# Kernel optimization log

Hardware: AMD Instinct MI355X
Metric: run time of the kernel (lower is better)

Reference implementation:

```python
import jax, jax.numpy as jnp
import numpy as np

IMAGE_SIZE = 1280
STRIDES = (8, 16, 32)
NUM_CLASSES = 80
BPC = 3  # boxes per cell
NMS_THRESH = 0.5
CONF_THRESH = 0.3
K_LEVEL = 1000
K_TOTAL = 3 * K_LEVEL
CLASS_OFFSET = 1.0e7  # shift boxes per class so cross-class IoU == 0 (== per-class NMS)
ANCHORS = np.array([[10,13],[16,30],[33,23],[30,61],[62,45],[59,119],
                    [116,90],[156,198],[373,326]], np.float32).reshape(3, 3, 2)

def level_anchors(level):
    f = IMAGE_SIZE // STRIDES[level]
    gy, gx = jnp.meshgrid(jnp.arange(f), jnp.arange(f), indexing='ij')
    xy = jnp.stack([gx, gy], -1).astype(jnp.float32).reshape(f * f, 1, 2)
    xy = jnp.broadcast_to(xy, (f * f, BPC, 2)).reshape(-1, 2)
    wh = jnp.broadcast_to(jnp.asarray(ANCHORS[level]), (f * f, BPC, 2)).reshape(-1, 2)
    return jnp.concatenate([xy, wh], -1)  # [M, 4]

def decode_boxes(anchors, reg, level):
    ctr = (jax.nn.sigmoid(reg[:, :2]) + anchors[:, :2]) * STRIDES[level]
    wh = jnp.exp(reg[:, 2:]) * anchors[:, 2:]
    return jnp.concatenate([ctr - wh * 0.5, ctr + wh * 0.5], -1)  # [M, 4] x1y1x2y2

def topk_level(obj, cls, reg, level):
    boxes = decode_boxes(level_anchors(level), reg, level)          # [M, 4]
    scores = jnp.sqrt(jax.nn.sigmoid(obj) * jax.nn.sigmoid(cls))    # [M, C]
    top_s, top_i = jax.lax.top_k(scores.reshape(-1), K_LEVEL)       # over M*C
    anchor_idx = top_i // NUM_CLASSES
    labels = top_i % NUM_CLASSES
    return top_s, labels, boxes[anchor_idx]

def nms_keep(boxes, scores, labels, valid):
    # Replicate source nms(): decoded x1y1x2y2 boxes are (re-)treated as cxcywh.
    b = jnp.concatenate([boxes[:, :2] - boxes[:, 2:] * 0.5,
                         boxes[:, :2] + boxes[:, 2:] * 0.5], -1)
    # class-aware: offset x-coords per class label
    off = labels.astype(jnp.float32) * CLASS_OFFSET
    b = b + off[:, None] * jnp.array([1.0, 0.0, 1.0, 0.0], b.dtype)
    x1, y1, x2, y2 = b[:, 0], b[:, 1], b[:, 2], b[:, 3]
    area = (x2 - x1) * (y2 - y1)
    xx1 = jnp.maximum(x1[:, None], x1[None, :])
    yy1 = jnp.maximum(y1[:, None], y1[None, :])
    xx2 = jnp.minimum(x2[:, None], x2[None, :])
    yy2 = jnp.minimum(y2[:, None], y2[None, :])
    inter = jnp.maximum(1e-10, xx2 - xx1) * jnp.maximum(1e-10, yy2 - yy1)
    iou = inter / (area[:, None] + area[None, :] - inter + 1e-14)   # [K, K]
    idx = jnp.arange(boxes.shape[0])
    def body(i, keep):
        sup = (iou[i] > NMS_THRESH) & (idx > i) & keep[i]
        return keep & ~sup
    return jax.lax.fori_loop(0, boxes.shape[0], body, valid)

def setup_inputs():
    key = jax.random.key(0)
    ks = jax.random.split(key, 9)
    d = {}
    for lvl, M in enumerate([76800, 19200, 4800]):
        d[f'obj{lvl}'] = jax.random.normal(ks[3 * lvl + 0], (M, 1), jnp.float32)
        d[f'cls{lvl}'] = jax.random.normal(ks[3 * lvl + 1], (M, NUM_CLASSES), jnp.float32)
        d[f'reg{lvl}'] = jax.random.normal(ks[3 * lvl + 2], (M, 4), jnp.float32)
    return d

def reference(obj0, cls0, reg0, obj1, cls1, reg1, obj2, cls2, reg2):
    levels = [(obj0, cls0, reg0), (obj1, cls1, reg1), (obj2, cls2, reg2)]
    ss, ls, bs = zip(*[topk_level(o, c, r, lvl) for lvl, (o, c, r) in enumerate(levels)])
    scores = jnp.concatenate(ss)        # [K_TOTAL]
    labels = jnp.concatenate(ls)
    boxes = jnp.concatenate(bs)         # [K_TOTAL, 4]
    # global sort by score (descending) so greedy NMS visits in score order
    scores, order = jax.lax.top_k(scores, K_TOTAL)
    labels = labels[order]
    boxes = boxes[order]
    valid = scores > CONF_THRESH
    keep = nms_keep(boxes, scores, labels, valid)
    out_boxes = jnp.where(keep[:, None], boxes, 0.0)
    out_scores = jnp.where(keep, scores, 0.0)
    out_labels = jnp.where(keep, labels, -1).astype(jnp.int32)
    return out_boxes, out_scores, out_labels, keep
```

## Files before the change

kernel.cpp:

```cpp
#include <hip/hip_runtime.h>
#include <hip/hip_bf16.h>
#include <math.h>

typedef unsigned int u32;
typedef unsigned long long u64;

#define NCLS 80
#define KLVL 1000
#define CAP  8192
#define TARGET 1100u

#define OFF_CAND   0u
#define OFF_HIST   196608u
#define OFF_CNT    221184u
#define OFF_GFLAT  221216u
#define OFF_GSB    233216u
#define OFF_SRT    245216u
#define OFF_QX1    257216u
#define OFF_QY1    269216u
#define OFF_QX2    281216u
#define OFF_QY2    293216u
#define OFF_AREA   305216u
#define OFF_SCORE  317216u
#define OFF_LABEL  329216u
#define OFF_VALID  341216u
#define OFF_KEEP   353216u
#define OFF_OBOX   365216u
#define OFF_SOBJ   413216u

__constant__ float cANCH[3][3][2] = {
  {{10.f,13.f},{16.f,30.f},{33.f,23.f}},
  {{30.f,61.f},{62.f,45.f},{59.f,119.f}},
  {{116.f,90.f},{156.f,198.f},{373.f,326.f}}
};

__device__ __forceinline__ float sig_fast(float x) {
  return 1.0f / (1.0f + __expf(-x));
}
__device__ __forceinline__ float sig_crit(float x) {
#pragma clang fp contract(off)
  double e = exp(-(double)x);
  float ef = (float)e;
  return 1.0f / (1.0f + ef);
}

__global__ __launch_bounds__(256) void kA(const float* __restrict__ o0,
                                          const float* __restrict__ o1,
                                          const float* __restrict__ o2,
                                          u32* __restrict__ hist,
                                          u32* __restrict__ cnt,
                                          u32* __restrict__ gsbits,
                                          u32* __restrict__ gflat,
                                          float* __restrict__ sobj) {
  int t = blockIdx.x * 256 + threadIdx.x;
  if (t < 3 * 2048) hist[t] = 0u;
  if (t < 8) cnt[t] = 0u;
  if (t < 3000) { gsbits[t] = 0u; gflat[t] = 0u; }
  if (t < 100800) {
    const float* o; int a;
    if (t < 76800)      { o = o0; a = t; }
    else if (t < 96000) { o = o1; a = t - 76800; }
    else                { o = o2; a = t - 96000; }
    sobj[t] = sig_fast(o[a]);
  }
}

__device__ __forceinline__ void block_map(int bid, int& l, int& e0, int& sob) {
  if (bid < 6000)      { l = 0; e0 = bid * 1024;          sob = 0; }
  else if (bid < 7500) { l = 1; e0 = (bid - 6000) * 1024; sob = 76800; }
  else                 { l = 2; e0 = (bid - 7500) * 1024; sob = 96000; }
}

__global__ __launch_bounds__(256) void kB(const float* __restrict__ c0,
                                          const float* __restrict__ c1,
                                          const float* __restrict__ c2,
                                          const float* __restrict__ sobj,
                                          u32* __restrict__ ghist) {
  __shared__ u32 lh[2048];
  for (int i = threadIdx.x; i < 2048; i += 256) lh[i] = 0u;
  __syncthreads();
  int l, e0, sob; block_map(blockIdx.x, l, e0, sob);
  const float* cls = (l == 0) ? c0 : (l == 1) ? c1 : c2;
  int e = e0 + threadIdx.x * 4;
  float4 cv = *(const float4*)(cls + e);
  float so = sobj[sob + e / 80];
  float cc[4] = {cv.x, cv.y, cv.z, cv.w};
#pragma unroll
  for (int k = 0; k < 4; k++) {
    float p = so * sig_fast(cc[k]);
    atomicAdd(&lh[__float_as_uint(p) >> 19], 1u);
  }
  __syncthreads();
  for (int i = threadIdx.x; i < 2048; i += 256) {
    u32 v = lh[i];
    if (v) atomicAdd(&ghist[l * 2048 + i], v);
  }
}

__global__ void k2(const u32* __restrict__ ghist, u32* __restrict__ cnt) {
  int l = threadIdx.x;
  if (l < 3) {
    u32 c = 0; int b = 2047;
    for (; b >= 0; --b) { c += ghist[l * 2048 + b]; if (c >= TARGET) break; }
    if (b < 0) b = 0;
    cnt[4 + l] = ((u32)b) << 19;
  }
}

__global__ __launch_bounds__(256) void k3(const float* __restrict__ c0,
                                          const float* __restrict__ c1,
                                          const float* __restrict__ c2,
                                          const float* __restrict__ o0,
                                          const float* __restrict__ o1,
                                          const float* __restrict__ o2,
                                          const float* __restrict__ sobj,
                                          u32* __restrict__ cnt,
                                          u64* __restrict__ cand) {
  int l, e0, sob; block_map(blockIdx.x, l, e0, sob);
  const float* cls = (l == 0) ? c0 : (l == 1) ? c1 : c2;
  const float* obj = (l == 0) ? o0 : (l == 1) ? o1 : o2;
  u32 T = cnt[4 + l];
  u32 Tm = (T > 64u) ? (T - 64u) : 0u;
  int e = e0 + threadIdx.x * 4;
  float4 cv = *(const float4*)(cls + e);
  int a = e / 80;
  float so = sobj[sob + a];
  float cc[4] = {cv.x, cv.y, cv.z, cv.w};
#pragma unroll
  for (int k = 0; k < 4; k++) {
    float pch = so * sig_fast(cc[k]);
    if (__float_as_uint(pch) >= Tm) {
      float soe = sig_crit(obj[a]);
      float sce = sig_crit(cc[k]);
      float p = soe * sce;
      u32 bits = __float_as_uint(p);
      if (bits >= T) {
        u32 slot = atomicAdd(&cnt[l], 1u);
        if (slot < CAP) {
          float s = __fsqrt_rn(p);
          u64 key = ((u64)__float_as_uint(s) << 32) | (u32)(~((u32)(e + k)));
          cand[(size_t)l * CAP + slot] = key;
        }
      }
    }
  }
}

__global__ __launch_bounds__(256) void r1(const u64* __restrict__ cand,
                                          const u32* __restrict__ cnt,
                                          u32* __restrict__ gsbits,
                                          u32* __restrict__ gflat) {
  int l = blockIdx.x >> 5;
  int b = blockIdx.x & 31;
  u32 n = cnt[l]; if (n > CAP) n = CAP;
  if ((u32)(b * 256) >= n) return;
  const u64* base = cand + (size_t)l * CAP;
  __shared__ u64 S[1024];
  u32 idx = (u32)(b * 256 + threadIdx.x);
  u64 mykey = (idx < n) ? base[idx] : 0ull;
  u32 rank = 0;
  for (u32 c0 = 0; c0 < n; c0 += 1024) {
    u32 m = (n - c0 < 1024u) ? (n - c0) : 1024u;
    __syncthreads();
    for (u32 i = threadIdx.x; i < 1024; i += 256)
      S[i] = (c0 + i < n) ? base[c0 + i] : 0ull;
    __syncthreads();
    if (idx < n) {
#pragma unroll 4
      for (u32 i = 0; i < m; ++i) rank += (S[i] > mykey) ? 1u : 0u;
    }
  }
  if (idx < n && rank < KLVL) {
    gsbits[l * KLVL + rank] = (u32)(mykey >> 32);
    gflat [l * KLVL + rank] = ~((u32)mykey);
  }
}

__global__ __launch_bounds__(256) void r2(const u32* __restrict__ gsbits,
                                          u32* __restrict__ srt) {
  __shared__ u64 S[3000];
  int t = blockIdx.x * 256 + threadIdx.x;
  for (u32 i = threadIdx.x; i < 3000; i += 256)
    S[i] = (((u64)gsbits[i]) << 32) | (u32)(~i);
  __syncthreads();
  if (t < 3000) {
    u64 my = (((u64)gsbits[t]) << 32) | (u32)(~t);
    u32 rank = 0;
#pragma unroll 4
    for (u32 i = 0; i < 3000; ++i) rank += (S[i] > my) ? 1u : 0u;
    srt[rank] = (u32)t;
  }
}

__global__ __launch_bounds__(256) void k6(const float* __restrict__ r0,
                                          const float* __restrict__ r1_,
                                          const float* __restrict__ r2_,
                                          const u32* __restrict__ srt,
                                          const u32* __restrict__ gsbits,
                                          const u32* __restrict__ gflat,
                                          float* __restrict__ qx1, float* __restrict__ qy1,
                                          float* __restrict__ qx2, float* __restrict__ qy2,
                                          float* __restrict__ area,
                                          float* __restrict__ score,
                                          u32* __restrict__ label,
                                          u32* __restrict__ valid,
                                          u32* __restrict__ keep,
                                          float* __restrict__ obox) {
#pragma clang fp contract(off)
  int r = blockIdx.x * 256 + threadIdx.x;
  if (r >= 3000) return;
  u32 gpos = srt[r];
  int l = (int)(gpos / 1000u);
  u32 flat = gflat[gpos];
  float sc = __uint_as_float(gsbits[gpos]);
  int a = (int)(flat / NCLS), c = (int)(flat % NCLS);
  int cell = a / 3, bi = a % 3;
  int f = (l == 0) ? 160 : (l == 1) ? 80 : 40;
  float stride = (float)(8 << l);
  float gx = (float)(cell % f), gy = (float)(cell / f);
  const float* rp = ((l == 0) ? r0 : (l == 1) ? r1_ : r2_) + (size_t)a * 4;
  float t0 = rp[0], t1 = rp[1], t2 = rp[2], t3 = rp[3];
  float sx = 1.0f / (1.0f + expf(-t0));
  float sy = 1.0f / (1.0f + expf(-t1));
  float w = expf(t2) * cANCH[l][bi][0];
  float h = expf(t3) * cANCH[l][bi][1];
  float cx = (sx + gx) * stride;
  float cy = (sy + gy) * stride;
  float hw = w * 0.5f, hh = h * 0.5f;
  float x1 = cx - hw, y1 = cy - hh, x2 = cx + hw, y2 = cy + hh;
  obox[r * 4 + 0] = x1; obox[r * 4 + 1] = y1;
  obox[r * 4 + 2] = x2; obox[r * 4 + 3] = y2;
  float hx2 = x2 * 0.5f, hy2 = y2 * 0.5f;
  float bx1 = x1 - hx2, by1 = y1 - hy2, bx2 = x1 + hx2, by2 = y1 + hy2;
  float off = (float)c * 1e7f;
  float a1 = bx1 + off, a2 = bx2 + off;
  qx1[r] = a1; qy1[r] = by1; qx2[r] = a2; qy2[r] = by2;
  area[r] = (a2 - a1) * (by2 - by1);
  score[r] = sc; label[r] = (u32)c;
  valid[r] = (sc > 0.3f) ? 1u : 0u;
  keep[r] = 0u;
}

#define CAPC 1024
__global__ __launch_bounds__(64) void k7(const float* __restrict__ qx1,
                                         const float* __restrict__ qy1,
                                         const float* __restrict__ qx2,
                                         const float* __restrict__ qy2,
                                         const float* __restrict__ area,
                                         const u32* __restrict__ label,
                                         const u32* __restrict__ valid,
                                         u32* __restrict__ keep) {
#pragma clang fp contract(off)
  __shared__ u32 LIST[CAPC];
  __shared__ float X1[CAPC], Y1[CAPC], X2[CAPC], Y2[CAPC], AR[CAPC];
  __shared__ u32 KP[CAPC];
  u32 c = blockIdx.x;
  int lane = threadIdx.x;
  u32 n = 0;
  for (int base = 0; base < 3000; base += 64) {
    int j = base + lane;
    bool m = false;
    if (j < 3000) m = (label[j] == c) && (valid[j] != 0u);
    u64 mask = __ballot(m ? 1 : 0);
    u32 pos = n + (u32)__popcll(mask & ((1ull << lane) - 1ull));
    if (m && pos < CAPC) {
      LIST[pos] = (u32)j;
      X1[pos] = qx1[j]; Y1[pos] = qy1[j];
      X2[pos] = qx2[j]; Y2[pos] = qy2[j];
      AR[pos] = area[j]; KP[pos] = 1u;
    }
    n += (u32)__popcll(mask);
  }
  if (n > CAPC) n = CAPC;
  __syncthreads();
  for (u32 i = 0; i < n; ++i) {
    if (KP[i]) {
      float xi1 = X1[i], yi1 = Y1[i], xi2 = X2[i], yi2 = Y2[i], ai = AR[i];
      for (u32 j = i + 1 + (u32)lane; j < n; j += 64) {
        if (KP[j]) {
          float xx1 = fmaxf(xi1, X1[j]);
          float yy1 = fmaxf(yi1, Y1[j]);
          float xx2 = fminf(xi2, X2[j]);
          float yy2 = fminf(yi2, Y2[j]);
          float iw = xx2 - xx1, ih = yy2 - yy1;
          float inter = fmaxf(1e-10f, iw) * fmaxf(1e-10f, ih);
          float den = ai + AR[j] - inter + 1e-14f;
          if (inter / den > 0.5f) KP[j] = 0u;
        }
      }
    }
    __syncthreads();
  }
  for (u32 j = (u32)lane; j < n; j += 64) keep[LIST[j]] = KP[j];
}

__global__ __launch_bounds__(256) void k8(const float* __restrict__ obox,
                                          const float* __restrict__ score,
                                          const u32* __restrict__ label,
                                          const u32* __restrict__ keep,
                                          float* __restrict__ out) {
  int r = blockIdx.x * 256 + threadIdx.x;
  if (r >= 3000) return;
  bool k = keep[r] != 0u;
  float4 b;
  if (k) b = *(const float4*)(obox + (size_t)r * 4);
  else   b = make_float4(0.f, 0.f, 0.f, 0.f);
  ((float4*)out)[r] = b;
  out[12000 + r] = k ? score[r] : 0.0f;
  out[15000 + r] = k ? (float)(int)label[r] : -1.0f;
  out[18000 + r] = k ? 1.0f : 0.0f;
}

extern "C" void kernel_launch(void* const* d_in, const int* in_sizes, int n_in,
                              void* d_out, int out_size, void* d_ws, size_t ws_size,
                              hipStream_t stream) {
  const float* obj0 = (const float*)d_in[0];
  const float* cls0 = (const float*)d_in[1];
  const float* reg0 = (const float*)d_in[2];
  const float* obj1 = (const float*)d_in[3];
  const float* cls1 = (const float*)d_in[4];
  const float* reg1 = (const float*)d_in[5];
  const float* obj2 = (const float*)d_in[6];
  const float* cls2 = (const float*)d_in[7];
  const float* reg2 = (const float*)d_in[8];
  char* ws = (char*)d_ws;
  u64* cand   = (u64*)(ws + OFF_CAND);
  u32* hist   = (u32*)(ws + OFF_HIST);
  u32* cnt    = (u32*)(ws + OFF_CNT);
  u32* gflat  = (u32*)(ws + OFF_GFLAT);
  u32* gsbits = (u32*)(ws + OFF_GSB);
  u32* srt    = (u32*)(ws + OFF_SRT);
  float* qx1  = (float*)(ws + OFF_QX1);
  float* qy1  = (float*)(ws + OFF_QY1);
  float* qx2  = (float*)(ws + OFF_QX2);
  float* qy2  = (float*)(ws + OFF_QY2);
  float* area = (float*)(ws + OFF_AREA);
  float* score= (float*)(ws + OFF_SCORE);
  u32* label  = (u32*)(ws + OFF_LABEL);
  u32* valid  = (u32*)(ws + OFF_VALID);
  u32* keep   = (u32*)(ws + OFF_KEEP);
  float* obox = (float*)(ws + OFF_OBOX);
  float* sobj = (float*)(ws + OFF_SOBJ);
  float* out  = (float*)d_out;

  kA<<<394, 256, 0, stream>>>(obj0, obj1, obj2, hist, cnt, gsbits, gflat, sobj);
  kB<<<7875, 256, 0, stream>>>(cls0, cls1, cls2, sobj, hist);
  k2<<<1, 64, 0, stream>>>(hist, cnt);
  k3<<<7875, 256, 0, stream>>>(cls0, cls1, cls2, obj0, obj1, obj2, sobj, cnt, cand);
  r1<<<96, 256, 0, stream>>>(cand, cnt, gsbits, gflat);
  r2<<<12, 256, 0, stream>>>(gsbits, srt);
  k6<<<12, 256, 0, stream>>>(reg0, reg1, reg2, srt, gsbits, gflat,
                             qx1, qy1, qx2, qy2, area, score, label, valid, keep, obox);
  k7<<<80, 64, 0, stream>>>(qx1, qy1, qx2, qy2, area, label, valid, keep);
  k8<<<12, 256, 0, stream>>>(obox, score, label, keep, out);
}
```

Baseline: 409.2 us.

## Sample histogram threshold, fuse sort/gather/output kernels, drop sigmoid-obj precompute

```diff
diff --git a/kernel.cpp b/kernel.cpp
--- a/kernel.cpp
+++ b/kernel.cpp
@@ -8,25 +8,22 @@
 #define NCLS 80
 #define KLVL 1000
 #define CAP  8192
-#define TARGET 1100u
+#define TARGET_S 160u
 
 #define OFF_CAND   0u
 #define OFF_HIST   196608u
 #define OFF_CNT    221184u
 #define OFF_GFLAT  221216u
 #define OFF_GSB    233216u
-#define OFF_SRT    245216u
-#define OFF_QX1    257216u
-#define OFF_QY1    269216u
-#define OFF_QX2    281216u
-#define OFF_QY2    293216u
-#define OFF_AREA   305216u
-#define OFF_SCORE  317216u
-#define OFF_LABEL  329216u
-#define OFF_VALID  341216u
-#define OFF_KEEP   353216u
-#define OFF_OBOX   365216u
-#define OFF_SOBJ   413216u
+#define OFF_QX1    245216u
+#define OFF_QY1    257216u
+#define OFF_QX2    269216u
+#define OFF_QY2    281216u
+#define OFF_AREA   293216u
+#define OFF_SCORE  305216u
+#define OFF_LABEL  317216u
+#define OFF_VALID  329216u
+#define OFF_OBOX   341216u
 
 __constant__ float cANCH[3][3][2] = {
   {{10.f,13.f},{16.f,30.f},{33.f,23.f}},
@@ -44,46 +41,35 @@
   return 1.0f / (1.0f + ef);
 }
 
-__global__ __launch_bounds__(256) void kA(const float* __restrict__ o0,
-                                          const float* __restrict__ o1,
-                                          const float* __restrict__ o2,
-                                          u32* __restrict__ hist,
+__global__ __launch_bounds__(256) void kA(u32* __restrict__ hist,
                                           u32* __restrict__ cnt,
                                           u32* __restrict__ gsbits,
-                                          u32* __restrict__ gflat,
-                                          float* __restrict__ sobj) {
+                                          u32* __restrict__ gflat) {
   int t = blockIdx.x * 256 + threadIdx.x;
-  if (t < 3 * 2048) hist[t] = 0u;
-  if (t < 8) cnt[t] = 0u;
-  if (t < 3000) { gsbits[t] = 0u; gflat[t] = 0u; }
-  if (t < 100800) {
-    const float* o; int a;
-    if (t < 76800)      { o = o0; a = t; }
-    else if (t < 96000) { o = o1; a = t - 76800; }
-    else                { o = o2; a = t - 96000; }
-    sobj[t] = sig_fast(o[a]);
-  }
-}
-
-__device__ __forceinline__ void block_map(int bid, int& l, int& e0, int& sob) {
-  if (bid < 6000)      { l = 0; e0 = bid * 1024;          sob = 0; }
-  else if (bid < 7500) { l = 1; e0 = (bid - 6000) * 1024; sob = 76800; }
-  else                 { l = 2; e0 = (bid - 7500) * 1024; sob = 96000; }
-}
-
-__global__ __launch_bounds__(256) void kB(const float* __restrict__ c0,
-                                          const float* __restrict__ c1,
-                                          const float* __restrict__ c2,
-                                          const float* __restrict__ sobj,
-                                          u32* __restrict__ ghist) {
+  if (t < 6144) hist[t] = 0u;
+  else if (t < 6152) cnt[t - 6144] = 0u;
+  else if (t < 9152) gsbits[t - 6152] = 0u;
+  else if (t < 12152) gflat[t - 9152] = 0u;
+}
+
+__global__ __launch_bounds__(256) void kB_s(const float* __restrict__ c0,
+                                            const float* __restrict__ c1,
+                                            const float* __restrict__ c2,
+                                            const float* __restrict__ o0,
+                                            const float* __restrict__ o1,
+                                            const float* __restrict__ o2,
+                                            u32* __restrict__ ghist) {
   __shared__ u32 lh[2048];
   for (int i = threadIdx.x; i < 2048; i += 256) lh[i] = 0u;
   __syncthreads();
-  int l, e0, sob; block_map(blockIdx.x, l, e0, sob);
-  const float* cls = (l == 0) ? c0 : (l == 1) ? c1 : c2;
+  int bid = blockIdx.x;
+  int l, e0; const float* cls; const float* obj;
+  if (bid < 375)      { l = 0; e0 = (bid * 16 + 8) * 1024;         cls = c0; obj = o0; }
+  else if (bid < 469) { l = 1; e0 = ((bid - 375) * 16 + 8) * 1024; cls = c1; obj = o1; }
+  else                { l = 2; e0 = ((bid - 469) * 16 + 8) * 1024; cls = c2; obj = o2; }
   int e = e0 + threadIdx.x * 4;
   float4 cv = *(const float4*)(cls + e);
-  float so = sobj[sob + e / 80];
+  float so = sig_fast(obj[e / 80]);
   float cc[4] = {cv.x, cv.y, cv.z, cv.w};
 #pragma unroll
   for (int k = 0; k < 4; k++) {
@@ -97,14 +83,39 @@
   }
 }
 
-__global__ void k2(const u32* __restrict__ ghist, u32* __restrict__ cnt) {
-  int l = threadIdx.x;
-  if (l < 3) {
-    u32 c = 0; int b = 2047;
-    for (; b >= 0; --b) { c += ghist[l * 2048 + b]; if (c >= TARGET) break; }
-    if (b < 0) b = 0;
-    cnt[4 + l] = ((u32)b) << 19;
-  }
+__global__ __launch_bounds__(64) void k2(const u32* __restrict__ ghist,
+                                         u32* __restrict__ cnt) {
+  int l = blockIdx.x;
+  int lane = threadIdx.x;
+  const u32* h = ghist + l * 2048;
+  int top = 2047 - lane * 32;
+  u32 s = 0;
+#pragma unroll
+  for (int i = 0; i < 32; i++) s += h[top - i];
+  u32 pre = s;
+#pragma unroll
+  for (int off = 1; off < 64; off <<= 1) {
+    u32 o = __shfl_up(pre, off);
+    if (lane >= off) pre += o;
+  }
+  u64 m = __ballot(pre >= TARGET_S);
+  if (m == 0ull) { if (lane == 0) cnt[4 + l] = 0u; return; }
+  int sel = __ffsll((long long)m) - 1;
+  if (lane == sel) {
+    u32 c = pre - s;
+    u32 bb = 0u;
+    for (int i = 0; i < 32; i++) {
+      c += h[top - i];
+      if (c >= TARGET_S) { bb = (u32)(top - i); break; }
+    }
+    cnt[4 + l] = bb << 19;
+  }
+}
+
+__device__ __forceinline__ void block_map(int bid, int& l, int& e0) {
+  if (bid < 6000)      { l = 0; e0 = bid * 1024; }
+  else if (bid < 7500) { l = 1; e0 = (bid - 6000) * 1024; }
+  else                 { l = 2; e0 = (bid - 7500) * 1024; }
 }
 
 __global__ __launch_bounds__(256) void k3(const float* __restrict__ c0,
@@ -113,10 +124,9 @@
                                           const float* __restrict__ o0,
                                           const float* __restrict__ o1,
                                           const float* __restrict__ o2,
-                                          const float* __restrict__ sobj,
                                           u32* __restrict__ cnt,
                                           u64* __restrict__ cand) {
-  int l, e0, sob; block_map(blockIdx.x, l, e0, sob);
+  int l, e0; block_map(blockIdx.x, l, e0);
   const float* cls = (l == 0) ? c0 : (l == 1) ? c1 : c2;
   const float* obj = (l == 0) ? o0 : (l == 1) ? o1 : o2;
   u32 T = cnt[4 + l];
@@ -124,7 +134,7 @@
   int e = e0 + threadIdx.x * 4;
   float4 cv = *(const float4*)(cls + e);
   int a = e / 80;
-  float so = sobj[sob + a];
+  float so = sig_fast(obj[a]);
   float cc[4] = {cv.x, cv.y, cv.z, cv.w};
 #pragma unroll
   for (int k = 0; k < 4; k++) {
@@ -153,66 +163,50 @@
   int l = blockIdx.x >> 5;
   int b = blockIdx.x & 31;
   u32 n = cnt[l]; if (n > CAP) n = CAP;
-  if ((u32)(b * 256) >= n) return;
+  u32 idx = (u32)(b * 256 + threadIdx.x);
+  if (idx >= n) return;
   const u64* base = cand + (size_t)l * CAP;
-  __shared__ u64 S[1024];
-  u32 idx = (u32)(b * 256 + threadIdx.x);
-  u64 mykey = (idx < n) ? base[idx] : 0ull;
+  u64 my = base[idx];
   u32 rank = 0;
-  for (u32 c0 = 0; c0 < n; c0 += 1024) {
-    u32 m = (n - c0 < 1024u) ? (n - c0) : 1024u;
-    __syncthreads();
-    for (u32 i = threadIdx.x; i < 1024; i += 256)
-      S[i] = (c0 + i < n) ? base[c0 + i] : 0ull;
-    __syncthreads();
-    if (idx < n) {
-#pragma unroll 4
-      for (u32 i = 0; i < m; ++i) rank += (S[i] > mykey) ? 1u : 0u;
-    }
-  }
-  if (idx < n && rank < KLVL) {
-    gsbits[l * KLVL + rank] = (u32)(mykey >> 32);
-    gflat [l * KLVL + rank] = ~((u32)mykey);
-  }
-}
-
-__global__ __launch_bounds__(256) void r2(const u32* __restrict__ gsbits,
-                                          u32* __restrict__ srt) {
-  __shared__ u64 S[3000];
+#pragma unroll 8
+  for (u32 i = 0; i < n; ++i) rank += (base[i] > my) ? 1u : 0u;
+  if (rank < KLVL) {
+    gsbits[l * KLVL + rank] = (u32)(my >> 32);
+    gflat [l * KLVL + rank] = ~((u32)my);
+  }
+}
+
+__global__ __launch_bounds__(256) void rk6(const float* __restrict__ r0,
+                                           const float* __restrict__ r1_,
+                                           const float* __restrict__ r2_,
+                                           const u32* __restrict__ gsbits,
+                                           const u32* __restrict__ gflat,
+                                           float* __restrict__ qx1, float* __restrict__ qy1,
+                                           float* __restrict__ qx2, float* __restrict__ qy2,
+                                           float* __restrict__ area,
+                                           float* __restrict__ score,
+                                           u32* __restrict__ label,
+                                           u32* __restrict__ valid,
+                                           float* __restrict__ obox,
+                                           float* __restrict__ out) {
+#pragma clang fp contract(off)
   int t = blockIdx.x * 256 + threadIdx.x;
-  for (u32 i = threadIdx.x; i < 3000; i += 256)
-    S[i] = (((u64)gsbits[i]) << 32) | (u32)(~i);
-  __syncthreads();
-  if (t < 3000) {
-    u64 my = (((u64)gsbits[t]) << 32) | (u32)(~t);
-    u32 rank = 0;
-#pragma unroll 4
-    for (u32 i = 0; i < 3000; ++i) rank += (S[i] > my) ? 1u : 0u;
-    srt[rank] = (u32)t;
-  }
-}
-
-__global__ __launch_bounds__(256) void k6(const float* __restrict__ r0,
-                                          const float* __restrict__ r1_,
-                                          const float* __restrict__ r2_,
-                                          const u32* __restrict__ srt,
-                                          const u32* __restrict__ gsbits,
-                                          const u32* __restrict__ gflat,
-                                          float* __restrict__ qx1, float* __restrict__ qy1,
-                                          float* __restrict__ qx2, float* __restrict__ qy2,
-                                          float* __restrict__ area,
-                                          float* __restrict__ score,
-                                          u32* __restrict__ label,
-                                          u32* __restrict__ valid,
-                                          u32* __restrict__ keep,
-                                          float* __restrict__ obox) {
-#pragma clang fp contract(off)
-  int r = blockIdx.x * 256 + threadIdx.x;
-  if (r >= 3000) return;
-  u32 gpos = srt[r];
-  int l = (int)(gpos / 1000u);
-  u32 flat = gflat[gpos];
-  float sc = __uint_as_float(gsbits[gpos]);
+  if (t >= 3000) return;
+  ((float4*)out)[t] = make_float4(0.f, 0.f, 0.f, 0.f);
+  out[12000 + t] = 0.0f;
+  out[15000 + t] = -1.0f;
+  out[18000 + t] = 0.0f;
+  u32 myb = gsbits[t];
+  u64 my = (((u64)myb) << 32) | (u32)(~t);
+  u32 rank = 0;
+#pragma unroll 8
+  for (int i = 0; i < 3000; ++i) {
+    u64 k = (((u64)gsbits[i]) << 32) | (u32)(~i);
+    rank += (k > my) ? 1u : 0u;
+  }
+  int l = t / 1000;
+  u32 flat = gflat[t];
+  float sc = __uint_as_float(myb);
   int a = (int)(flat / NCLS), c = (int)(flat % NCLS);
   int cell = a / 3, bi = a % 3;
   int f = (l == 0) ? 160 : (l == 1) ? 80 : 40;
@@ -228,17 +222,15 @@
   float cy = (sy + gy) * stride;
   float hw = w * 0.5f, hh = h * 0.5f;
   float x1 = cx - hw, y1 = cy - hh, x2 = cx + hw, y2 = cy + hh;
-  obox[r * 4 + 0] = x1; obox[r * 4 + 1] = y1;
-  obox[r * 4 + 2] = x2; obox[r * 4 + 3] = y2;
+  ((float4*)obox)[rank] = make_float4(x1, y1, x2, y2);
   float hx2 = x2 * 0.5f, hy2 = y2 * 0.5f;
   float bx1 = x1 - hx2, by1 = y1 - hy2, bx2 = x1 + hx2, by2 = y1 + hy2;
   float off = (float)c * 1e7f;
   float a1 = bx1 + off, a2 = bx2 + off;
-  qx1[r] = a1; qy1[r] = by1; qx2[r] = a2; qy2[r] = by2;
-  area[r] = (a2 - a1) * (by2 - by1);
-  score[r] = sc; label[r] = (u32)c;
-  valid[r] = (sc > 0.3f) ? 1u : 0u;
-  keep[r] = 0u;
+  qx1[rank] = a1; qy1[rank] = by1; qx2[rank] = a2; qy2[rank] = by2;
+  area[rank] = (a2 - a1) * (by2 - by1);
+  score[rank] = sc; label[rank] = (u32)c;
+  valid[rank] = (sc > 0.3f) ? 1u : 0u;
 }
 
 #define CAPC 1024
@@ -247,9 +239,11 @@
                                          const float* __restrict__ qx2,
                                          const float* __restrict__ qy2,
                                          const float* __restrict__ area,
+                                         const float* __restrict__ score,
                                          const u32* __restrict__ label,
                                          const u32* __restrict__ valid,
-                                         u32* __restrict__ keep) {
+                                         const float* __restrict__ obox,
+                                         float* __restrict__ out) {
 #pragma clang fp contract(off)
   __shared__ u32 LIST[CAPC];
   __shared__ float X1[CAPC], Y1[CAPC], X2[CAPC], Y2[CAPC], AR[CAPC];
@@ -291,24 +285,16 @@
     }
     __syncthreads();
   }
-  for (u32 j = (u32)lane; j < n; j += 64) keep[LIST[j]] = KP[j];
-}
-
-__global__ __launch_bounds__(256) void k8(const float* __restrict__ obox,
-                                          const float* __restrict__ score,
-                                          const u32* __restrict__ label,
-                                          const u32* __restrict__ keep,
-                                          float* __restrict__ out) {
-  int r = blockIdx.x * 256 + threadIdx.x;
-  if (r >= 3000) return;
-  bool k = keep[r] != 0u;
-  float4 b;
-  if (k) b = *(const float4*)(obox + (size_t)r * 4);
-  else   b = make_float4(0.f, 0.f, 0.f, 0.f);
-  ((float4*)out)[r] = b;
-  out[12000 + r] = k ? score[r] : 0.0f;
-  out[15000 + r] = k ? (float)(int)label[r] : -1.0f;
-  out[18000 + r] = k ? 1.0f : 0.0f;
+  for (u32 j = (u32)lane; j < n; j += 64) {
+    if (KP[j]) {
+      u32 r = LIST[j];
+      float4 bx = ((const float4*)obox)[r];
+      ((float4*)out)[r] = bx;
+      out[12000 + r] = score[r];
+      out[15000 + r] = (float)(int)c;
+      out[18000 + r] = 1.0f;
+    }
+  }
 }
 
 extern "C" void kernel_launch(void* const* d_in, const int* in_sizes, int n_in,
@@ -329,7 +315,6 @@
   u32* cnt    = (u32*)(ws + OFF_CNT);
   u32* gflat  = (u32*)(ws + OFF_GFLAT);
   u32* gsbits = (u32*)(ws + OFF_GSB);
-  u32* srt    = (u32*)(ws + OFF_SRT);
   float* qx1  = (float*)(ws + OFF_QX1);
   float* qy1  = (float*)(ws + OFF_QY1);
   float* qx2  = (float*)(ws + OFF_QX2);
@@ -338,19 +323,15 @@
   float* score= (float*)(ws + OFF_SCORE);
   u32* label  = (u32*)(ws + OFF_LABEL);
   u32* valid  = (u32*)(ws + OFF_VALID);
-  u32* keep   = (u32*)(ws + OFF_KEEP);
   float* obox = (float*)(ws + OFF_OBOX);
-  float* sobj = (float*)(ws + OFF_SOBJ);
   float* out  = (float*)d_out;
 
-  kA<<<394, 256, 0, stream>>>(obj0, obj1, obj2, hist, cnt, gsbits, gflat, sobj);
-  kB<<<7875, 256, 0, stream>>>(cls0, cls1, cls2, sobj, hist);
-  k2<<<1, 64, 0, stream>>>(hist, cnt);
-  k3<<<7875, 256, 0, stream>>>(cls0, cls1, cls2, obj0, obj1, obj2, sobj, cnt, cand);
+  kA<<<48, 256, 0, stream>>>(hist, cnt, gsbits, gflat);
+  kB_s<<<492, 256, 0, stream>>>(cls0, cls1, cls2, obj0, obj1, obj2, hist);
+  k2<<<3, 64, 0, stream>>>(hist, cnt);
+  k3<<<7875, 256, 0, stream>>>(cls0, cls1, cls2, obj0, obj1, obj2, cnt, cand);
   r1<<<96, 256, 0, stream>>>(cand, cnt, gsbits, gflat);
-  r2<<<12, 256, 0, stream>>>(gsbits, srt);
-  k6<<<12, 256, 0, stream>>>(reg0, reg1, reg2, srt, gsbits, gflat,
-                             qx1, qy1, qx2, qy2, area, score, label, valid, keep, obox);
-  k7<<<80, 64, 0, stream>>>(qx1, qy1, qx2, qy2, area, label, valid, keep);
-  k8<<<12, 256, 0, stream>>>(obox, score, label, keep, out);
-}
+  rk6<<<12, 256, 0, stream>>>(reg0, reg1, reg2, gsbits, gflat,
+                              qx1, qy1, qx2, qy2, area, score, label, valid, obox, out);
+  k7<<<80, 64, 0, stream>>>(qx1, qy1, qx2, qy2, area, score, label, valid, obox, out);
+}
```

After: 428.6 us. 4.7% more time.
